# Kernel optimization log

Measured on AMD Instinct MI355X. Metric: run time of the kernel, lower is better.

## Reference

```python
import jax, jax.numpy as jnp
import numpy as np

B, C, L, H = 4, 128, 4096, 4
GROUPS, EPS = 32, 1e-5


def group_norm(x, gamma, beta):
    # x: [B, C, L]; normalize per (batch, group) over (C//G, L)
    b, c, l = x.shape
    xg = x.reshape(b, GROUPS, c // GROUPS, l)
    mu = jnp.mean(xg, axis=(2, 3), keepdims=True)
    var = jnp.var(xg, axis=(2, 3), keepdims=True)
    xn = ((xg - mu) * jax.lax.rsqrt(var + EPS)).reshape(b, c, l)
    return xn * gamma[None, :, None] + beta[None, :, None]


def setup_inputs() -> dict:
    key = jax.random.key(0)
    k1, k2, k3 = jax.random.split(key, 3)
    return {
        "x": jax.random.normal(k1, (B, C, L), dtype=jnp.float32),
        "w_qkv": jax.random.normal(k2, (3 * C, C), dtype=jnp.float32) * 0.02,
        "w_proj": jax.random.normal(k3, (C, C), dtype=jnp.float32) * 0.02,
        "b_proj": jnp.zeros((C,), dtype=jnp.float32),
        "gn_gamma": jnp.ones((C,), dtype=jnp.float32),
        "gn_beta": jnp.zeros((C,), dtype=jnp.float32),
    }


def reference(x, w_qkv, w_proj, b_proj, gn_gamma, gn_beta):
    b, c, l = x.shape
    hd = c // H
    h = group_norm(x, gn_gamma, gn_beta)
    # 1x1 conv == channel matmul: [B, 3C, L]
    qkv = jnp.einsum('oc,bcl->bol', w_qkv, h)
    # torch reshape(B*H, 3C/H, L).chunk(3, dim=1): per-head contiguous slices
    qkv = qkv.reshape(b, H, 3 * hd, l)
    q, k, v = qkv[:, :, :hd], qkv[:, :, hd:2 * hd], qkv[:, :, 2 * hd:]
    scale = 1.0 / np.sqrt(np.sqrt(hd)).astype(np.float32)
    attn = jnp.einsum('bhct,bhcs->bhts', q * scale, k * scale)
    attn = jax.nn.softmax(attn, axis=-1)
    o = jnp.einsum('bhts,bhcs->bhct', attn, v).reshape(b, c, l)
    o = jnp.einsum('oc,bcl->bol', w_proj, o) + b_proj[None, :, None]
    return o + x
```

## Files before the change

### kernel.cpp

```cpp
#include <hip/hip_runtime.h>
#include <hip/hip_bf16.h>
#include <cstdint>
#include <cstddef>


#define B_ 4
#define C_ 128
#define L_ 4096
#define H_ 4
#define HD_ 32
#define NG_ 32
#define CPG_ 4
#define EPS_ 1e-5f
#define QKSCALE_ 0.5050097650430367f

typedef __attribute__((ext_vector_type(8))) short bf16x8;
typedef __attribute__((ext_vector_type(8))) unsigned short u16x8;
typedef __attribute__((ext_vector_type(4))) float f32x4;
typedef __attribute__((ext_vector_type(2))) _Float16 f16x2;
typedef __attribute__((ext_vector_type(4))) _Float16 f16x4;

#if __has_builtin(__builtin_amdgcn_exp2f)
#define EXP2F(x) __builtin_amdgcn_exp2f(x)
#else
#define EXP2F(x) exp2f(x)
#endif

#define MFMA_PV(a, b, c) __builtin_amdgcn_mfma_f32_16x16x16f16((a), (b), (c), 0, 0, 0)

__device__ __forceinline__ float bu2f(unsigned short u) {
  return __builtin_bit_cast(float, (unsigned int)(((unsigned int)u) << 16));
}
__device__ __forceinline__ unsigned short f2bu(float f) {
  unsigned int u = __builtin_bit_cast(unsigned int, f);
  unsigned int r = (u + 0x7fffu + ((u >> 16) & 1u)) >> 16;
  return (unsigned short)r;
}
__device__ __forceinline__ float4 u42f4(ushort4 u) {
  return make_float4(bu2f(u.x), bu2f(u.y), bu2f(u.z), bu2f(u.w));
}
__device__ __forceinline__ unsigned int pkbf(float a, float b) {
  return (unsigned int)f2bu(a) | ((unsigned int)f2bu(b) << 16);
}
__device__ __forceinline__ f16x2 pkhf2(float a, float b) {
#if __has_builtin(__builtin_amdgcn_cvt_pkrtz)
  return __builtin_bit_cast(f16x2, __builtin_amdgcn_cvt_pkrtz(a, b));
#else
  f16x2 r;
  r[0] = (_Float16)a;
  r[1] = (_Float16)b;
  return r;
#endif
}
__device__ __forceinline__ unsigned int pkhf(float a, float b) {
  return __builtin_bit_cast(unsigned int, pkhf2(a, b));
}

__device__ __forceinline__ bool detect_fast(const ushort* x) {
  __shared__ int flag_s;
  int t = threadIdx.x;
  if (t < 64) {
    int e = (x[t] >> 7) & 0xFF;
    unsigned long long m = __ballot((e < 64) || (e > 192));
    if (t == 0) flag_s = (__popcll(m) > 4) ? 1 : 0;
  }
  __syncthreads();
  return flag_s != 0;
}

__device__ __forceinline__ float4 ldx4(const void* x, size_t idx, bool f32) {
  if (f32) return *((const float4*)x + (idx >> 2));
  ushort4 u = *((const ushort4*)x + (idx >> 2));
  return u42f4(u);
}

__global__ __launch_bounds__(256) void gn_stats(const void* __restrict__ x,
                                                const void* __restrict__ wq,
                                                const void* __restrict__ wp,
                                                const void* __restrict__ bp,
                                                const void* __restrict__ gm,
                                                const void* __restrict__ bt,
                                                ushort* __restrict__ wq_b,
                                                ushort* __restrict__ wp_b,
                                                float* __restrict__ bp_f,
                                                float2* __restrict__ gn_ab) {
  bool f32 = detect_fast((const ushort*)x);
  int blk = blockIdx.x;
  int t = threadIdx.x;

  if (blk >= 128) {
    int i0 = ((blk - 128) * 256 + t) * 8;
#pragma unroll
    for (int k = 0; k < 8; ++k) {
      int i = i0 + k;
      if (i >= 65664) break;
      if (i < 49152) {
        wq_b[i] = f32 ? f2bu(((const float*)wq)[i]) : ((const ushort*)wq)[i];
      } else if (i < 65536) {
        int off = i - 49152;
        wp_b[off] = f32 ? f2bu(((const float*)wp)[off]) : ((const ushort*)wp)[off];
      } else {
        int off = i - 65536;
        bp_f[off] = f32 ? ((const float*)bp)[off] : bu2f(((const ushort*)bp)[off]);
      }
    }
    return;
  }

  int b = blk >> 5, g = blk & 31;
  size_t base = ((size_t)b * C_ + (size_t)g * CPG_) * L_;

  float s = 0.f, ss = 0.f;
#pragma unroll
  for (int i = 0; i < 16; ++i) {
    size_t e = base + i * 1024 + t * 4;
    float4 f = ldx4(x, e, f32);
    s += f.x + f.y + f.z + f.w;
    ss += f.x * f.x + f.y * f.y + f.z * f.z + f.w * f.w;
  }
#pragma unroll
  for (int m = 32; m >= 1; m >>= 1) {
    s += __shfl_xor(s, m, 64);
    ss += __shfl_xor(ss, m, 64);
  }
  __shared__ float red[4][2];
  int wv = t >> 6;
  if ((t & 63) == 0) { red[wv][0] = s; red[wv][1] = ss; }
  __syncthreads();
  float ts = red[0][0] + red[1][0] + red[2][0] + red[3][0];
  float tss = red[0][1] + red[1][1] + red[2][1] + red[3][1];
  float mu = ts * (1.0f / 16384.0f);
  float var = tss * (1.0f / 16384.0f) - mu * mu;
  float rs = rsqrtf(var + EPS_);

  if (t < CPG_) {
    int gi = g * CPG_ + t;
    float ga = f32 ? ((const float*)gm)[gi] : bu2f(((const ushort*)gm)[gi]);
    float be = f32 ? ((const float*)bt)[gi] : bu2f(((const ushort*)bt)[gi]);
    gn_ab[b * C_ + gi] = make_float2(ga * rs, be - mu * ga * rs);
  }
}

__global__ __launch_bounds__(256) void qkv_kernel(const ushort* __restrict__ wq_b,
                                                  const void* __restrict__ x,
                                                  const float2* __restrict__ gn_ab,
                                                  ushort* __restrict__ Qt,
                                                  ushort* __restrict__ Kt,
                                                  ushort* __restrict__ Vb) {
  bool f32 = detect_fast((const ushort*)x);
  __shared__ alignas(16) ushort Hs[64][136];
  __shared__ alignas(16) float Ls[64][69];

  int lx = blockIdx.x, oz = blockIdx.y, b = blockIdx.z;
  int t = threadIdx.x;
  int w = t >> 6, lane = t & 63, l16 = lane & 15, q = lane >> 4, q8 = q * 8;

  {
    int u = t & 63, lh = (t >> 6) * 16;
    int c0 = 2 * u;
    float2 ab0 = gn_ab[b * C_ + c0];
    float2 ab1 = gn_ab[b * C_ + c0 + 1];
    size_t xo = ((size_t)b * C_ + c0) * L_ + (size_t)lx * 64 + lh;
#pragma unroll
    for (int j = 0; j < 4; ++j) {
      float4 f0 = ldx4(x, xo + j * 4, f32);
      float4 f1 = ldx4(x, xo + L_ + j * 4, f32);
      float n0[4] = {f0.x * ab0.x + ab0.y, f0.y * ab0.x + ab0.y,
                     f0.z * ab0.x + ab0.y, f0.w * ab0.x + ab0.y};
      float n1[4] = {f1.x * ab1.x + ab1.y, f1.y * ab1.x + ab1.y,
                     f1.z * ab1.x + ab1.y, f1.w * ab1.x + ab1.y};
#pragma unroll
      for (int k = 0; k < 4; ++k)
        *(unsigned int*)&Hs[lh + j * 4 + k][c0] = pkbf(n0[k], n1[k]);
    }
  }
  __syncthreads();

  for (int j = 0; j < 2; ++j) {
    int oy = oz * 2 + j;
    const ushort* wg = wq_b + (size_t)(oy * 64 + w * 16 + l16) * C_;

    f32x4 acc[4] = {{0.f, 0.f, 0.f, 0.f}, {0.f, 0.f, 0.f, 0.f},
                    {0.f, 0.f, 0.f, 0.f}, {0.f, 0.f, 0.f, 0.f}};
#pragma unroll
    for (int kc = 0; kc < 4; ++kc) {
      bf16x8 aw = *(const bf16x8*)(wg + kc * 32 + q8);
#pragma unroll
      for (int nb = 0; nb < 4; ++nb) {
        bf16x8 bh = *(const bf16x8*)&Hs[nb * 16 + l16][kc * 32 + q8];
        acc[nb] = __builtin_amdgcn_mfma_f32_16x16x32_bf16(aw, bh, acc[nb], 0, 0, 0);
      }
    }
    __syncthreads();
#pragma unroll
    for (int nb = 0; nb < 4; ++nb)
#pragma unroll
      for (int r = 0; r < 4; ++r)
        Ls[nb * 16 + l16][w * 16 + 4 * q + r] = acc[nb][r];
    __syncthreads();

#pragma unroll
    for (int hhalf = 0; hhalf < 2; ++hhalf) {
      int hh = oy * 2 + hhalf;
      int type = hh % 3, head = hh / 3;
      size_t bh = (size_t)b * H_ + head;
      if (type == 2) {
        int c_loc = t >> 3, l8 = (t & 7) * 8;
        float v[8];
#pragma unroll
        for (int jj = 0; jj < 8; ++jj) v[jj] = Ls[l8 + jj][hhalf * 32 + c_loc];
        uint4 u;
        u.x = pkhf(v[0], v[1]);
        u.y = pkhf(v[2], v[3]);
        u.z = pkhf(v[4], v[5]);
        u.w = pkhf(v[6], v[7]);
        *(uint4*)(Vb + (bh * 32 + c_loc) * L_ + (size_t)lx * 64 + l8) = u;
      } else {
        ushort* dst = type ? Kt : Qt;
        int l = t >> 2, seg = (t & 3) * 8;
        const float* src = &Ls[l][hhalf * 32 + seg];
        uint4 u;
        u.x = pkbf(src[0] * QKSCALE_, src[1] * QKSCALE_);
        u.y = pkbf(src[2] * QKSCALE_, src[3] * QKSCALE_);
        u.z = pkbf(src[4] * QKSCALE_, src[5] * QKSCALE_);
        u.w = pkbf(src[6] * QKSCALE_, src[7] * QKSCALE_);
        *(uint4*)(dst + ((bh * L_) + lx * 64 + l) * 32 + seg) = u;
      }
    }
  }
}

__global__ __launch_bounds__(256) void attn_kernel(const ushort* __restrict__ Qt,
                                                   const ushort* __restrict__ Kt,
                                                   const ushort* __restrict__ Vb,
                                                   ushort* __restrict__ ot) {
  __shared__ alignas(16) ushort Ks[2][4096];
  __shared__ alignas(16) ushort Vs[2][32][136];

  int t = threadIdx.x;
  int w = t >> 6, lane = t & 63, l16 = lane & 15, q = lane >> 4;
  int tq0 = blockIdx.x * 128;
  int bh = blockIdx.y;
  int b = bh >> 2, head = bh & 3;
  const ushort* Qg = Qt + ((size_t)bh * L_ + tq0) * 32;
  const ushort* Kg = Kt + (size_t)bh * L_ * 32;
  const ushort* Vg = Vb + (size_t)bh * 32 * L_;

  int krow = (t & 15) | ((t >> 6) << 4);
  int kq8 = ((t >> 4) & 3) * 8;
  const ushort* kgp = Kg + (size_t)krow * 32 + kq8;
  int vc = t >> 3, vsl = (t & 7) * 8;
  const ushort* vgp = Vg + (size_t)vc * L_ + vsl;
  int trow = w * 16 + l16;
  int q8 = q * 8, q4 = q * 4;

  bf16x8 qfrag0 = *(const bf16x8*)(Qg + (size_t)trow * 32 + q8);
  bf16x8 qfrag1 = *(const bf16x8*)(Qg + (size_t)(64 + trow) * 32 + q8);
  f16x4 ones;
#pragma unroll
  for (int i = 0; i < 4; ++i) ones[i] = (_Float16)1.0f;

  *(uint4*)&Ks[0][t * 8] = *(const uint4*)kgp;
  *(uint4*)&Ks[0][2048 + t * 8] = *(const uint4*)(kgp + 2048);
  *(uint4*)&Vs[0][vc][vsl] = *(const uint4*)vgp;
  *(uint4*)&Vs[0][vc][64 + vsl] = *(const uint4*)(vgp + 64);
  __syncthreads();

  f32x4 aA0 = {0.f, 0.f, 0.f, 0.f}, aB0 = {0.f, 0.f, 0.f, 0.f};
  f32x4 aA1 = {0.f, 0.f, 0.f, 0.f}, aB1 = {0.f, 0.f, 0.f, 0.f};
  f32x4 aL0 = {0.f, 0.f, 0.f, 0.f}, aL1 = {0.f, 0.f, 0.f, 0.f};
  const ushort* kg_n = kgp + 4096;
  const ushort* vg_n = vgp + 128;

#pragma unroll 2
  for (int it = 0; it < 32; ++it) {
    int bc = it & 1;
    if (it < 31) {
      *(uint4*)&Ks[bc ^ 1][t * 8] = *(const uint4*)kg_n;
      *(uint4*)&Ks[bc ^ 1][2048 + t * 8] = *(const uint4*)(kg_n + 2048);
      *(uint4*)&Vs[bc ^ 1][vc][vsl] = *(const uint4*)vg_n;
      *(uint4*)&Vs[bc ^ 1][vc][64 + vsl] = *(const uint4*)(vg_n + 64);
      kg_n += 4096;
      vg_n += 128;
    }

#pragma unroll
    for (int hh2 = 0; hh2 < 2; ++hh2) {
      const ushort* kf = &Ks[bc][hh2 * 2048 + lane * 8];
      bf16x8 ak0 = *(const bf16x8*)(kf);
      bf16x8 ak1 = *(const bf16x8*)(kf + 512);
      bf16x8 ak2 = *(const bf16x8*)(kf + 1024);
      bf16x8 ak3 = *(const bf16x8*)(kf + 1536);
      f32x4 z = {0.f, 0.f, 0.f, 0.f};
      f32x4 sf0[4], sf1[4];
      sf0[0] = __builtin_amdgcn_mfma_f32_16x16x32_bf16(ak0, qfrag0, z, 0, 0, 0);
      sf0[1] = __builtin_amdgcn_mfma_f32_16x16x32_bf16(ak1, qfrag0, z, 0, 0, 0);
      sf0[2] = __builtin_amdgcn_mfma_f32_16x16x32_bf16(ak2, qfrag0, z, 0, 0, 0);
      sf0[3] = __builtin_amdgcn_mfma_f32_16x16x32_bf16(ak3, qfrag0, z, 0, 0, 0);
      sf1[0] = __builtin_amdgcn_mfma_f32_16x16x32_bf16(ak0, qfrag1, z, 0, 0, 0);
      sf1[1] = __builtin_amdgcn_mfma_f32_16x16x32_bf16(ak1, qfrag1, z, 0, 0, 0);
      sf1[2] = __builtin_amdgcn_mfma_f32_16x16x32_bf16(ak2, qfrag1, z, 0, 0, 0);
      sf1[3] = __builtin_amdgcn_mfma_f32_16x16x32_bf16(ak3, qfrag1, z, 0, 0, 0);

#pragma unroll
      for (int n = 0; n < 4; ++n) {
        f16x4 va0 = *(const f16x4*)&Vs[bc][l16][hh2 * 64 + n * 16 + q4];
        f16x4 va1 = *(const f16x4*)&Vs[bc][16 + l16][hh2 * 64 + n * 16 + q4];
        {
          float p0 = EXP2F(sf0[n][0]);
          float p1 = EXP2F(sf0[n][1]);
          float p2 = EXP2F(sf0[n][2]);
          float p3 = EXP2F(sf0[n][3]);
          f16x2 e01 = pkhf2(p0, p1);
          f16x2 e23 = pkhf2(p2, p3);
          f16x4 pb = __builtin_shufflevector(e01, e23, 0, 1, 2, 3);
          aA0 = MFMA_PV(va0, pb, aA0);
          aB0 = MFMA_PV(va1, pb, aB0);
          aL0 = MFMA_PV(ones, pb, aL0);
        }
        {
          float p0 = EXP2F(sf1[n][0]);
          float p1 = EXP2F(sf1[n][1]);
          float p2 = EXP2F(sf1[n][2]);
          float p3 = EXP2F(sf1[n][3]);
          f16x2 e01 = pkhf2(p0, p1);
          f16x2 e23 = pkhf2(p2, p3);
          f16x4 pb = __builtin_shufflevector(e01, e23, 0, 1, 2, 3);
          aA1 = MFMA_PV(va0, pb, aA1);
          aB1 = MFMA_PV(va1, pb, aB1);
          aL1 = MFMA_PV(ones, pb, aL1);
        }
      }
    }
    __syncthreads();
  }

  float inv0 = 1.0f / aL0[0];
  float inv1 = 1.0f / aL1[0];

  __syncthreads();
  ushort* Ep = &Ks[0][0];
#pragma unroll
  for (int r = 0; r < 2; ++r) {
    *(unsigned int*)&Ep[trow * 40 + q4 + 2 * r] =
        pkbf(aA0[2 * r] * inv0, aA0[2 * r + 1] * inv0);
    *(unsigned int*)&Ep[trow * 40 + 16 + q4 + 2 * r] =
        pkbf(aB0[2 * r] * inv0, aB0[2 * r + 1] * inv0);
    *(unsigned int*)&Ep[(64 + trow) * 40 + q4 + 2 * r] =
        pkbf(aA1[2 * r] * inv1, aA1[2 * r + 1] * inv1);
    *(unsigned int*)&Ep[(64 + trow) * 40 + 16 + q4 + 2 * r] =
        pkbf(aB1[2 * r] * inv1, aB1[2 * r + 1] * inv1);
  }
  __syncthreads();
  {
    int row = t >> 2, seg = (t & 3) * 8;
#pragma unroll
    for (int p = 0; p < 2; ++p) {
      *(uint4*)(ot + ((size_t)b * L_ + tq0 + p * 64 + row) * C_ + head * 32 + seg) =
          *(const uint4*)&Ep[(p * 64 + row) * 40 + seg];
    }
  }
}

__global__ __launch_bounds__(256) void proj_kernel(const ushort* __restrict__ wp_b,
                                                   const float* __restrict__ bias,
                                                   const void* __restrict__ x,
                                                   const ushort* __restrict__ ot,
                                                   void* __restrict__ out) {
  bool f32 = detect_fast((const ushort*)x);
  __shared__ alignas(16) float Ls[64][37];

  int lx = blockIdx.x, oy = blockIdx.y, b = blockIdx.z;
  int t = threadIdx.x;
  int w = t >> 6, lane = t & 63, l16 = lane & 15, q = lane >> 4, q8 = q * 8;

  const ushort* wg = wp_b + (size_t)(oy * 64 + w * 16 + l16) * C_;
  const ushort* og = ot + ((size_t)b * L_ + (size_t)lx * 32) * C_;

  f32x4 acc[2] = {{0.f, 0.f, 0.f, 0.f}, {0.f, 0.f, 0.f, 0.f}};
#pragma unroll
  for (int kc = 0; kc < 4; ++kc) {
    bf16x8 aw = *(const bf16x8*)(wg + kc * 32 + q8);
#pragma unroll
    for (int nb = 0; nb < 2; ++nb) {
      bf16x8 bo = *(const bf16x8*)(og + (size_t)(nb * 16 + l16) * C_ + kc * 32 + q8);
      acc[nb] = __builtin_amdgcn_mfma_f32_16x16x32_bf16(aw, bo, acc[nb], 0, 0, 0);
    }
  }
#pragma unroll
  for (int nb = 0; nb < 2; ++nb)
#pragma unroll
    for (int r = 0; r < 4; ++r)
      Ls[w * 16 + 4 * q + r][nb * 16 + l16] = acc[nb][r];
  __syncthreads();

  {
    int o_loc = t >> 2, ls0 = (t & 3) * 8;
    float bv = bias[oy * 64 + o_loc];
    size_t off = ((size_t)b * C_ + oy * 64 + o_loc) * L_ + (size_t)lx * 32 + ls0;
#pragma unroll
    for (int jj = 0; jj < 2; ++jj) {
      float4 xf = ldx4(x, off + jj * 4, f32);
      const float* sp = &Ls[o_loc][ls0 + jj * 4];
      float4 r = make_float4(sp[0] + bv + xf.x, sp[1] + bv + xf.y,
                             sp[2] + bv + xf.z, sp[3] + bv + xf.w);
      if (f32) {
        *(float4*)((float*)out + off + jj * 4) = r;
      } else {
        *(ushort4*)((ushort*)out + off + jj * 4) =
            make_ushort4(f2bu(r.x), f2bu(r.y), f2bu(r.z), f2bu(r.w));
      }
    }
  }
}

extern "C" void kernel_launch(void* const* d_in, const int* in_sizes, int n_in,
                              void* d_out, int out_size, void* d_ws, size_t ws_size,
                              hipStream_t stream) {
  const void* x      = d_in[0];
  const void* w_qkv  = d_in[1];
  const void* w_proj = d_in[2];
  const void* b_proj = d_in[3];
  const void* gamma  = d_in[4];
  const void* beta   = d_in[5];

  char* wsb = (char*)d_ws;
  ushort* wq_b  = (ushort*)(wsb + 0);
  ushort* wp_b  = (ushort*)(wsb + 98304);
  float*  bp_f  = (float*)(wsb + 131072);
  float2* gn_ab = (float2*)(wsb + 131584);
  ushort* Qt    = (ushort*)(wsb + 8388608);
  ushort* Kt    = (ushort*)(wsb + 12582912);
  ushort* Vb    = (ushort*)(wsb + 16777216);
  ushort* ot    = (ushort*)(wsb + 20971520);

  gn_stats<<<dim3(161), dim3(256), 0, stream>>>(x, w_qkv, w_proj, b_proj, gamma, beta,
                                                wq_b, wp_b, bp_f, gn_ab);
  qkv_kernel<<<dim3(L_ / 64, 3, B_), dim3(256), 0, stream>>>(wq_b, x, gn_ab, Qt, Kt, Vb);
  attn_kernel<<<dim3(L_ / 128, B_ * H_), dim3(256), 0, stream>>>(Qt, Kt, Vb, ot);
  proj_kernel<<<dim3(L_ / 32, C_ / 64, B_), dim3(256), 0, stream>>>(wp_b, bp_f, x, ot, d_out);
}
```

Before: 151.7 us.

## Split attention key range in two and merge partial sums in projection

Attention now splits the key/value sequence into two halves across a new grid dimension, doubling the block count from 512 to 1024. Each half writes unnormalized fp32 partial outputs and row sums to workspace. The projection kernel adds the two partials, normalizes, and converts to bf16 before its MFMA. The split is safe without a running max because the softmax never subtracted one. It raises parallelism and occupancy on the many-CU GPU, at the cost of extra fp32 traffic (two partial buffers) and some extra work in the projection kernel.

```diff
diff --git a/kernel.cpp b/kernel.cpp
--- a/kernel.cpp
+++ b/kernel.cpp
@@ -233,18 +233,20 @@
 __global__ __launch_bounds__(256) void attn_kernel(const ushort* __restrict__ Qt,
                                                    const ushort* __restrict__ Kt,
                                                    const ushort* __restrict__ Vb,
-                                                   ushort* __restrict__ ot) {
+                                                   float* __restrict__ Pp,
+                                                   float* __restrict__ lsum) {
   __shared__ alignas(16) ushort Ks[2][4096];
   __shared__ alignas(16) ushort Vs[2][32][136];
 
   int t = threadIdx.x;
   int w = t >> 6, lane = t & 63, l16 = lane & 15, q = lane >> 4;
   int tq0 = blockIdx.x * 128;
-  int bh = blockIdx.y;
+  int sh = blockIdx.y;
+  int bh = blockIdx.z;
   int b = bh >> 2, head = bh & 3;
   const ushort* Qg = Qt + ((size_t)bh * L_ + tq0) * 32;
-  const ushort* Kg = Kt + (size_t)bh * L_ * 32;
-  const ushort* Vg = Vb + (size_t)bh * 32 * L_;
+  const ushort* Kg = Kt + ((size_t)bh * L_ + (size_t)sh * 2048) * 32;
+  const ushort* Vg = Vb + (size_t)bh * 32 * L_ + (size_t)sh * 2048;
 
   int krow = (t & 15) | ((t >> 6) << 4);
   int kq8 = ((t >> 4) & 3) * 8;
@@ -273,9 +275,9 @@
   const ushort* vg_n = vgp + 128;
 
 #pragma unroll 2
-  for (int it = 0; it < 32; ++it) {
+  for (int it = 0; it < 16; ++it) {
     int bc = it & 1;
-    if (it < 31) {
+    if (it < 15) {
       *(uint4*)&Ks[bc ^ 1][t * 8] = *(const uint4*)kg_n;
       *(uint4*)&Ks[bc ^ 1][2048 + t * 8] = *(const uint4*)(kg_n + 2048);
       *(uint4*)&Vs[bc ^ 1][vc][vsl] = *(const uint4*)vg_n;
@@ -335,37 +337,45 @@
     __syncthreads();
   }
 
-  float inv0 = 1.0f / aL0[0];
-  float inv1 = 1.0f / aL1[0];
-
-  __syncthreads();
-  ushort* Ep = &Ks[0][0];
-#pragma unroll
-  for (int r = 0; r < 2; ++r) {
-    *(unsigned int*)&Ep[trow * 40 + q4 + 2 * r] =
-        pkbf(aA0[2 * r] * inv0, aA0[2 * r + 1] * inv0);
-    *(unsigned int*)&Ep[trow * 40 + 16 + q4 + 2 * r] =
-        pkbf(aB0[2 * r] * inv0, aB0[2 * r + 1] * inv0);
-    *(unsigned int*)&Ep[(64 + trow) * 40 + q4 + 2 * r] =
-        pkbf(aA1[2 * r] * inv1, aA1[2 * r + 1] * inv1);
-    *(unsigned int*)&Ep[(64 + trow) * 40 + 16 + q4 + 2 * r] =
-        pkbf(aB1[2 * r] * inv1, aB1[2 * r + 1] * inv1);
-  }
-  __syncthreads();
   {
-    int row = t >> 2, seg = (t & 3) * 8;
-#pragma unroll
-    for (int p = 0; p < 2; ++p) {
-      *(uint4*)(ot + ((size_t)b * L_ + tq0 + p * 64 + row) * C_ + head * 32 + seg) =
-          *(const uint4*)&Ep[(p * 64 + row) * 40 + seg];
-    }
+    float* lp = lsum + ((size_t)sh * B_ * H_ + bh) * L_ + tq0;
+    if (q == 0) {
+      lp[trow] = aL0[0];
+      lp[64 + trow] = aL1[0];
+    }
+  }
+
+  float* Pb = Pp + (size_t)sh * ((size_t)B_ * L_ * C_) +
+              ((size_t)b * L_ + tq0) * C_ + head * 32;
+  float* Ep = (float*)&Ks[0][0];
+#pragma unroll
+  for (int p = 0; p < 2; ++p) {
+    f32x4 vA = p ? aA1 : aA0;
+    f32x4 vB = p ? aB1 : aB0;
+#pragma unroll
+    for (int r = 0; r < 4; ++r) {
+      Ep[trow * 36 + q4 + r] = vA[r];
+      Ep[trow * 36 + 16 + q4 + r] = vB[r];
+    }
+    __syncthreads();
+    {
+      int row = t >> 2, seg = (t & 3) * 8;
+      const float* sp = &Ep[row * 36 + seg];
+      float4 r0 = *(const float4*)sp;
+      float4 r1 = *(const float4*)(sp + 4);
+      float* dst = Pb + (size_t)(p * 64 + row) * C_ + seg;
+      *(float4*)dst = r0;
+      *(float4*)(dst + 4) = r1;
+    }
+    __syncthreads();
   }
 }
 
 __global__ __launch_bounds__(256) void proj_kernel(const ushort* __restrict__ wp_b,
                                                    const float* __restrict__ bias,
                                                    const void* __restrict__ x,
-                                                   const ushort* __restrict__ ot,
+                                                   const float* __restrict__ Pp,
+                                                   const float* __restrict__ lsum,
                                                    void* __restrict__ out) {
   bool f32 = detect_fast((const ushort*)x);
   __shared__ alignas(16) float Ls[64][37];
@@ -375,7 +385,18 @@
   int w = t >> 6, lane = t & 63, l16 = lane & 15, q = lane >> 4, q8 = q * 8;
 
   const ushort* wg = wp_b + (size_t)(oy * 64 + w * 16 + l16) * C_;
-  const ushort* og = ot + ((size_t)b * L_ + (size_t)lx * 32) * C_;
+  const float* og0 = Pp + ((size_t)b * L_ + (size_t)lx * 32) * C_;
+  const size_t HALF = (size_t)B_ * L_ * C_;
+  const size_t LHALF = (size_t)B_ * H_ * L_;
+
+  float inv[2][4];
+#pragma unroll
+  for (int nb = 0; nb < 2; ++nb)
+#pragma unroll
+    for (int kc = 0; kc < 4; ++kc) {
+      size_t li = ((size_t)b * H_ + kc) * L_ + (size_t)lx * 32 + nb * 16 + l16;
+      inv[nb][kc] = 1.0f / (lsum[li] + lsum[LHALF + li]);
+    }
 
   f32x4 acc[2] = {{0.f, 0.f, 0.f, 0.f}, {0.f, 0.f, 0.f, 0.f}};
 #pragma unroll
@@ -383,7 +404,18 @@
     bf16x8 aw = *(const bf16x8*)(wg + kc * 32 + q8);
 #pragma unroll
     for (int nb = 0; nb < 2; ++nb) {
-      bf16x8 bo = *(const bf16x8*)(og + (size_t)(nb * 16 + l16) * C_ + kc * 32 + q8);
+      const float* pf = og0 + (size_t)(nb * 16 + l16) * C_ + kc * 32 + q8;
+      float4 u0 = *(const float4*)pf;
+      float4 u1 = *(const float4*)(pf + 4);
+      float4 v0 = *(const float4*)(pf + HALF);
+      float4 v1 = *(const float4*)(pf + HALF + 4);
+      float s = inv[nb][kc];
+      uint4 pk;
+      pk.x = pkbf((u0.x + v0.x) * s, (u0.y + v0.y) * s);
+      pk.y = pkbf((u0.z + v0.z) * s, (u0.w + v0.w) * s);
+      pk.z = pkbf((u1.x + v1.x) * s, (u1.y + v1.y) * s);
+      pk.w = pkbf((u1.z + v1.z) * s, (u1.w + v1.w) * s);
+      bf16x8 bo = __builtin_bit_cast(bf16x8, pk);
       acc[nb] = __builtin_amdgcn_mfma_f32_16x16x32_bf16(aw, bo, acc[nb], 0, 0, 0);
     }
   }
@@ -429,14 +461,15 @@
   ushort* wp_b  = (ushort*)(wsb + 98304);
   float*  bp_f  = (float*)(wsb + 131072);
   float2* gn_ab = (float2*)(wsb + 131584);
+  float*  lsum  = (float*)(wsb + 139264);
   ushort* Qt    = (ushort*)(wsb + 8388608);
   ushort* Kt    = (ushort*)(wsb + 12582912);
   ushort* Vb    = (ushort*)(wsb + 16777216);
-  ushort* ot    = (ushort*)(wsb + 20971520);
+  float*  Pp    = (float*)(wsb + 20971520);
 
   gn_stats<<<dim3(161), dim3(256), 0, stream>>>(x, w_qkv, w_proj, b_proj, gamma, beta,
                                                 wq_b, wp_b, bp_f, gn_ab);
   qkv_kernel<<<dim3(L_ / 64, 3, B_), dim3(256), 0, stream>>>(wq_b, x, gn_ab, Qt, Kt, Vb);
-  attn_kernel<<<dim3(L_ / 128, B_ * H_), dim3(256), 0, stream>>>(Qt, Kt, Vb, ot);
-  proj_kernel<<<dim3(L_ / 32, C_ / 64, B_), dim3(256), 0, stream>>>(wp_b, bp_f, x, ot, d_out);
-}
+  attn_kernel<<<dim3(L_ / 128, 2, B_ * H_), dim3(256), 0, stream>>>(Qt, Kt, Vb, Pp, lsum);
+  proj_kernel<<<dim3(L_ / 32, C_ / 64, B_), dim3(256), 0, stream>>>(wp_b, bp_f, x, Pp, lsum, d_out);
+}
```

After: 154.6 us. Within noise of the previous version (+2.0%).

## Use direct global-to-LDS loads, 512 threads per attention block, swizzled V

Applied to the files above, without the earlier changes.

The attention kernel moves from 256 to 512 threads, so each wave handles one 16-row query tile instead of two, which halves accumulator register pressure and doubles the waves per block. K/V tiles are now loaded straight into LDS with global_load_lds instead of going through registers. V sits in an unpadded LDS buffer with an XOR swizzle to avoid bank conflicts, and the QK MFMAs are wrapped in setprio. The risk is more per-wave overhead and synchronisation cost, plus correctness questions about the async-load ordering relative to the barrier.

```diff
diff --git a/kernel.cpp b/kernel.cpp
--- a/kernel.cpp
+++ b/kernel.cpp
@@ -54,6 +54,12 @@
 }
 __device__ __forceinline__ unsigned int pkhf(float a, float b) {
   return __builtin_bit_cast(unsigned int, pkhf2(a, b));
+}
+
+__device__ __forceinline__ void gload16(const void* g, void* l) {
+  __builtin_amdgcn_global_load_lds(
+      (const __attribute__((address_space(1))) unsigned int*)g,
+      (__attribute__((address_space(3))) unsigned int*)l, 16, 0, 0);
 }
 
 __device__ __forceinline__ bool detect_fast(const ushort* x) {
@@ -230,15 +236,17 @@
   }
 }
 
-__global__ __launch_bounds__(256) void attn_kernel(const ushort* __restrict__ Qt,
+__global__ __launch_bounds__(512) void attn_kernel(const ushort* __restrict__ Qt,
                                                    const ushort* __restrict__ Kt,
                                                    const ushort* __restrict__ Vb,
                                                    ushort* __restrict__ ot) {
   __shared__ alignas(16) ushort Ks[2][4096];
-  __shared__ alignas(16) ushort Vs[2][32][136];
+  __shared__ alignas(16) ushort Vs[2][32][128];
 
   int t = threadIdx.x;
   int w = t >> 6, lane = t & 63, l16 = lane & 15, q = lane >> 4;
+  int q8 = q * 8, q4 = q * 4;
+  int trow = w * 16 + l16;
   int tq0 = blockIdx.x * 128;
   int bh = blockIdx.y;
   int b = bh >> 2, head = bh & 3;
@@ -246,119 +254,102 @@
   const ushort* Kg = Kt + (size_t)bh * L_ * 32;
   const ushort* Vg = Vb + (size_t)bh * 32 * L_;
 
-  int krow = (t & 15) | ((t >> 6) << 4);
-  int kq8 = ((t >> 4) & 3) * 8;
-  const ushort* kgp = Kg + (size_t)krow * 32 + kq8;
-  int vc = t >> 3, vsl = (t & 7) * 8;
-  const ushort* vgp = Vg + (size_t)vc * L_ + vsl;
-  int trow = w * 16 + l16;
-  int q8 = q * 8, q4 = q * 4;
-
-  bf16x8 qfrag0 = *(const bf16x8*)(Qg + (size_t)trow * 32 + q8);
-  bf16x8 qfrag1 = *(const bf16x8*)(Qg + (size_t)(64 + trow) * 32 + q8);
+  {
+  }
+  int j = t & 255;
+  int krow = ((j & 15) | ((j >> 6) << 4)) + ((t >> 8) << 6);
+  int kq8s = ((j >> 4) & 3) * 8;
+  const ushort* ksrc = Kg + (size_t)krow * 32 + kq8s;
+  int vr = t >> 4, vp = t & 15;
+  int vcsem = (vp & 8) | ((vp & 7) ^ (vr & 7));
+  const ushort* vsrc = Vg + (size_t)vr * L_ + vcsem * 8;
+
+  ushort* kA = (ushort*)Ks + (size_t)t * 8;
+  ushort* kB = kA + 4096;
+  ushort* vA = (ushort*)Vs + (size_t)t * 8;
+  ushort* vB = vA + 4096;
+
+  bf16x8 qfrag = *(const bf16x8*)(Qg + (size_t)trow * 32 + q8);
   f16x4 ones;
 #pragma unroll
   for (int i = 0; i < 4; ++i) ones[i] = (_Float16)1.0f;
 
-  *(uint4*)&Ks[0][t * 8] = *(const uint4*)kgp;
-  *(uint4*)&Ks[0][2048 + t * 8] = *(const uint4*)(kgp + 2048);
-  *(uint4*)&Vs[0][vc][vsl] = *(const uint4*)vgp;
-  *(uint4*)&Vs[0][vc][64 + vsl] = *(const uint4*)(vgp + 64);
-  __syncthreads();
-
-  f32x4 aA0 = {0.f, 0.f, 0.f, 0.f}, aB0 = {0.f, 0.f, 0.f, 0.f};
-  f32x4 aA1 = {0.f, 0.f, 0.f, 0.f}, aB1 = {0.f, 0.f, 0.f, 0.f};
-  f32x4 aL0 = {0.f, 0.f, 0.f, 0.f}, aL1 = {0.f, 0.f, 0.f, 0.f};
-  const ushort* kg_n = kgp + 4096;
-  const ushort* vg_n = vgp + 128;
-
-#pragma unroll 2
+  gload16(ksrc, kA);
+  gload16(vsrc, vA);
+  ksrc += 4096;
+  vsrc += 128;
+  __syncthreads();
+
+  f32x4 aA = {0.f, 0.f, 0.f, 0.f};
+  f32x4 aB = {0.f, 0.f, 0.f, 0.f};
+  f32x4 aL = {0.f, 0.f, 0.f, 0.f};
+
+  int flip = 0;
   for (int it = 0; it < 32; ++it) {
-    int bc = it & 1;
     if (it < 31) {
-      *(uint4*)&Ks[bc ^ 1][t * 8] = *(const uint4*)kg_n;
-      *(uint4*)&Ks[bc ^ 1][2048 + t * 8] = *(const uint4*)(kg_n + 2048);
-      *(uint4*)&Vs[bc ^ 1][vc][vsl] = *(const uint4*)vg_n;
-      *(uint4*)&Vs[bc ^ 1][vc][64 + vsl] = *(const uint4*)(vg_n + 64);
-      kg_n += 4096;
-      vg_n += 128;
-    }
+      gload16(ksrc, flip ? kA : kB);
+      gload16(vsrc, flip ? vA : vB);
+      ksrc += 4096;
+      vsrc += 128;
+    }
+    const ushort* kc = (const ushort*)Ks + (flip ? 4096 : 0);
+    const ushort* vc = (const ushort*)Vs + (flip ? 4096 : 0);
 
 #pragma unroll
     for (int hh2 = 0; hh2 < 2; ++hh2) {
-      const ushort* kf = &Ks[bc][hh2 * 2048 + lane * 8];
+      const ushort* kf = kc + hh2 * 2048 + lane * 8;
       bf16x8 ak0 = *(const bf16x8*)(kf);
       bf16x8 ak1 = *(const bf16x8*)(kf + 512);
       bf16x8 ak2 = *(const bf16x8*)(kf + 1024);
       bf16x8 ak3 = *(const bf16x8*)(kf + 1536);
       f32x4 z = {0.f, 0.f, 0.f, 0.f};
-      f32x4 sf0[4], sf1[4];
-      sf0[0] = __builtin_amdgcn_mfma_f32_16x16x32_bf16(ak0, qfrag0, z, 0, 0, 0);
-      sf0[1] = __builtin_amdgcn_mfma_f32_16x16x32_bf16(ak1, qfrag0, z, 0, 0, 0);
-      sf0[2] = __builtin_amdgcn_mfma_f32_16x16x32_bf16(ak2, qfrag0, z, 0, 0, 0);
-      sf0[3] = __builtin_amdgcn_mfma_f32_16x16x32_bf16(ak3, qfrag0, z, 0, 0, 0);
-      sf1[0] = __builtin_amdgcn_mfma_f32_16x16x32_bf16(ak0, qfrag1, z, 0, 0, 0);
-      sf1[1] = __builtin_amdgcn_mfma_f32_16x16x32_bf16(ak1, qfrag1, z, 0, 0, 0);
-      sf1[2] = __builtin_amdgcn_mfma_f32_16x16x32_bf16(ak2, qfrag1, z, 0, 0, 0);
-      sf1[3] = __builtin_amdgcn_mfma_f32_16x16x32_bf16(ak3, qfrag1, z, 0, 0, 0);
+      f32x4 sf[4];
+      __builtin_amdgcn_s_setprio(1);
+      sf[0] = __builtin_amdgcn_mfma_f32_16x16x32_bf16(ak0, qfrag, z, 0, 0, 0);
+      sf[1] = __builtin_amdgcn_mfma_f32_16x16x32_bf16(ak1, qfrag, z, 0, 0, 0);
+      sf[2] = __builtin_amdgcn_mfma_f32_16x16x32_bf16(ak2, qfrag, z, 0, 0, 0);
+      sf[3] = __builtin_amdgcn_mfma_f32_16x16x32_bf16(ak3, qfrag, z, 0, 0, 0);
+      __builtin_amdgcn_s_setprio(0);
 
 #pragma unroll
       for (int n = 0; n < 4; ++n) {
-        f16x4 va0 = *(const f16x4*)&Vs[bc][l16][hh2 * 64 + n * 16 + q4];
-        f16x4 va1 = *(const f16x4*)&Vs[bc][16 + l16][hh2 * 64 + n * 16 + q4];
-        {
-          float p0 = EXP2F(sf0[n][0]);
-          float p1 = EXP2F(sf0[n][1]);
-          float p2 = EXP2F(sf0[n][2]);
-          float p3 = EXP2F(sf0[n][3]);
-          f16x2 e01 = pkhf2(p0, p1);
-          f16x2 e23 = pkhf2(p2, p3);
-          f16x4 pb = __builtin_shufflevector(e01, e23, 0, 1, 2, 3);
-          aA0 = MFMA_PV(va0, pb, aA0);
-          aB0 = MFMA_PV(va1, pb, aB0);
-          aL0 = MFMA_PV(ones, pb, aL0);
-        }
-        {
-          float p0 = EXP2F(sf1[n][0]);
-          float p1 = EXP2F(sf1[n][1]);
-          float p2 = EXP2F(sf1[n][2]);
-          float p3 = EXP2F(sf1[n][3]);
-          f16x2 e01 = pkhf2(p0, p1);
-          f16x2 e23 = pkhf2(p2, p3);
-          f16x4 pb = __builtin_shufflevector(e01, e23, 0, 1, 2, 3);
-          aA1 = MFMA_PV(va0, pb, aA1);
-          aB1 = MFMA_PV(va1, pb, aB1);
-          aL1 = MFMA_PV(ones, pb, aL1);
-        }
+        int o = hh2 * 64 + n * 16 + q4;
+        int c = o >> 3;
+        int pch = (c & 8) | ((c & 7) ^ (l16 & 7));
+        const ushort* vrow = vc + pch * 8 + (q4 & 7);
+        f16x4 va0 = *(const f16x4*)(vrow + (size_t)l16 * 128);
+        f16x4 va1 = *(const f16x4*)(vrow + (size_t)(16 + l16) * 128);
+        float p0 = EXP2F(sf[n][0]);
+        float p1 = EXP2F(sf[n][1]);
+        float p2 = EXP2F(sf[n][2]);
+        float p3 = EXP2F(sf[n][3]);
+        f16x2 e01 = pkhf2(p0, p1);
+        f16x2 e23 = pkhf2(p2, p3);
+        f16x4 pb = __builtin_shufflevector(e01, e23, 0, 1, 2, 3);
+        aA = MFMA_PV(va0, pb, aA);
+        aB = MFMA_PV(va1, pb, aB);
+        aL = MFMA_PV(ones, pb, aL);
       }
     }
     __syncthreads();
-  }
-
-  float inv0 = 1.0f / aL0[0];
-  float inv1 = 1.0f / aL1[0];
-
-  __syncthreads();
-  ushort* Ep = &Ks[0][0];
+    flip ^= 1;
+  }
+
+  float inv = 1.0f / aL[0];
+
+  ushort* Ep = (ushort*)Ks;
 #pragma unroll
   for (int r = 0; r < 2; ++r) {
     *(unsigned int*)&Ep[trow * 40 + q4 + 2 * r] =
-        pkbf(aA0[2 * r] * inv0, aA0[2 * r + 1] * inv0);
+        pkbf(aA[2 * r] * inv, aA[2 * r + 1] * inv);
     *(unsigned int*)&Ep[trow * 40 + 16 + q4 + 2 * r] =
-        pkbf(aB0[2 * r] * inv0, aB0[2 * r + 1] * inv0);
-    *(unsigned int*)&Ep[(64 + trow) * 40 + q4 + 2 * r] =
-        pkbf(aA1[2 * r] * inv1, aA1[2 * r + 1] * inv1);
-    *(unsigned int*)&Ep[(64 + trow) * 40 + 16 + q4 + 2 * r] =
-        pkbf(aB1[2 * r] * inv1, aB1[2 * r + 1] * inv1);
+        pkbf(aB[2 * r] * inv, aB[2 * r + 1] * inv);
   }
   __syncthreads();
   {
     int row = t >> 2, seg = (t & 3) * 8;
-#pragma unroll
-    for (int p = 0; p < 2; ++p) {
-      *(uint4*)(ot + ((size_t)b * L_ + tq0 + p * 64 + row) * C_ + head * 32 + seg) =
-          *(const uint4*)&Ep[(p * 64 + row) * 40 + seg];
-    }
+    *(uint4*)(ot + ((size_t)b * L_ + tq0 + row) * C_ + head * 32 + seg) =
+        *(const uint4*)&Ep[row * 40 + seg];
   }
 }
 
@@ -437,6 +428,6 @@
   gn_stats<<<dim3(161), dim3(256), 0, stream>>>(x, w_qkv, w_proj, b_proj, gamma, beta,
                                                 wq_b, wp_b, bp_f, gn_ab);
   qkv_kernel<<<dim3(L_ / 64, 3, B_), dim3(256), 0, stream>>>(wq_b, x, gn_ab, Qt, Kt, Vb);
-  attn_kernel<<<dim3(L_ / 128, B_ * H_), dim3(256), 0, stream>>>(Qt, Kt, Vb, ot);
+  attn_kernel<<<dim3(L_ / 128, B_ * H_), dim3(512), 0, stream>>>(Qt, Kt, Vb, ot);
   proj_kernel<<<dim3(L_ / 32, C_ / 64, B_), dim3(256), 0, stream>>>(wp_b, bp_f, x, ot, d_out);
 }
```

After: 144.3 us. 1.05x faster.
